# Performance work log

Hardware: AMD Instinct MI355X
Metric: run time of the kernel (lower is better)

Reference implementation:

```python
import jax, jax.numpy as jnp
import numpy as np

DIM = 512
HEADS = 8
DIM_HEAD = 64
INNER = HEADS * DIM_HEAD  # 512
EPS = 1e-5
SCALE = DIM_HEAD ** (-0.5)


def setup_inputs() -> dict:
    key = jax.random.key(0)
    ks = jax.random.split(key, 12)
    B, S = 8, 1024
    x = jax.random.normal(ks[0], (B, DIM, S, 1), dtype=jnp.float32)
    # BatchNorm2d params (eval mode: running stats)
    bn_gamma = jax.random.normal(ks[1], (DIM,), dtype=jnp.float32) * 0.1 + 1.0
    bn_beta = jax.random.normal(ks[2], (DIM,), dtype=jnp.float32) * 0.1
    bn_mean = jax.random.normal(ks[3], (DIM,), dtype=jnp.float32) * 0.1
    bn_var = jax.random.uniform(ks[4], (DIM,), dtype=jnp.float32, minval=0.5, maxval=1.5)
    # 1x1 Conv2d == linear: weight [out, in], bias [out]
    def lin(k, out_d, in_d):
        kw, kb = jax.random.split(k)
        lim = 1.0 / np.sqrt(in_d)
        w = jax.random.uniform(kw, (out_d, in_d), dtype=jnp.float32, minval=-lim, maxval=lim)
        b = jax.random.uniform(kb, (out_d,), dtype=jnp.float32, minval=-lim, maxval=lim)
        return w, b
    wq, bq = lin(ks[5], INNER, DIM)
    wk, bk = lin(ks[6], INNER, DIM)
    wv, bv = lin(ks[7], INNER, DIM)
    wo, bo = lin(ks[8], DIM, INNER)
    return {"x": x, "bn_gamma": bn_gamma, "bn_beta": bn_beta,
            "bn_mean": bn_mean, "bn_var": bn_var,
            "wq": wq, "bq": bq, "wk": wk, "bk": bk,
            "wv": wv, "bv": bv, "wo": wo, "bo": bo}


def reference(x, bn_gamma, bn_beta, bn_mean, bn_var,
              wq, bq, wk, bk, wv, bv, wo, bo):
    B, C, S, _ = x.shape
    # BatchNorm2d (eval) over channel dim
    inv = jax.lax.rsqrt(bn_var + EPS)
    xn = (x - bn_mean[None, :, None, None]) * (bn_gamma * inv)[None, :, None, None] \
         + bn_beta[None, :, None, None]
    t = jnp.transpose(xn[..., 0], (0, 2, 1))  # [B, S, C]
    q = (t @ wq.T + bq).reshape(B, S, HEADS, DIM_HEAD)
    k = (t @ wk.T + bk).reshape(B, S, HEADS, DIM_HEAD)
    v = (t @ wv.T + bv).reshape(B, S, HEADS, DIM_HEAD)
    scores = jnp.einsum('bshd,bthd->bhst', q, k) * SCALE  # [B,H,S,S]
    attn = jax.nn.softmax(scores, axis=-1)
    o = jnp.einsum('bhst,bthd->bshd', attn, v).reshape(B, S, INNER)
    y = o @ wo.T + bo  # [B, S, C]
    return jnp.transpose(y, (0, 2, 1))[..., None]  # [B, C, S, 1]
```

## Files before the change

kernel.cpp:

```cpp
#include <hip/hip_runtime.h>
#include <stdint.h>

typedef __bf16 bf16;
typedef bf16 bf16x8 __attribute__((ext_vector_type(8)));
typedef bf16 bf16x4 __attribute__((ext_vector_type(4)));
typedef float f32x4 __attribute__((ext_vector_type(4)));

#define NB 8
#define NS 1024
#define NC 512
#define NH 8
#define ND 64

#define QSCALE 0.18033688011f

__device__ __forceinline__ void gload16(const void* g, void* l) {
  __builtin_amdgcn_global_load_lds(
      (const __attribute__((address_space(1))) void*)g,
      (__attribute__((address_space(3))) void*)l, 16, 0, 0);
}

__global__ __launch_bounds__(256) void bn_tr_kernel(
    const float* __restrict__ x, const float* __restrict__ gam,
    const float* __restrict__ bet, const float* __restrict__ mu,
    const float* __restrict__ var, bf16* __restrict__ t) {
  __shared__ float tile[32][33];
  const int b = blockIdx.z, c0 = blockIdx.y * 32, s0 = blockIdx.x * 32;
  const int tx = threadIdx.x, sj = tx & 31, ci = tx >> 5;
#pragma unroll
  for (int kk = 0; kk < 4; ++kk) {
    const int c = c0 + ci + (kk << 3);
    const float sc = gam[c] * rsqrtf(var[c] + 1e-5f);
    const float sh = bet[c] - mu[c] * sc;
    tile[ci + (kk << 3)][sj] = x[(size_t)(b * NC + c) * NS + s0 + sj] * sc + sh;
  }
  __syncthreads();
#pragma unroll
  for (int kk = 0; kk < 4; ++kk) {
    const int s = s0 + ci + (kk << 3);
    t[(size_t)(b * NS + s) * NC + c0 + sj] = (bf16)tile[sj][ci + (kk << 3)];
  }
}

__global__ __launch_bounds__(256) void wconv_kernel(
    const float* __restrict__ wq, const float* __restrict__ wk,
    const float* __restrict__ wv, const float* __restrict__ wo,
    bf16* __restrict__ wqb, bf16* __restrict__ wkb, bf16* __restrict__ wvb,
    bf16* __restrict__ wob) {
  const int i = (blockIdx.x * 256 + threadIdx.x) * 4;
  float4 a = *(const float4*)(&wq[i]);
  float4 b = *(const float4*)(&wk[i]);
  float4 c = *(const float4*)(&wv[i]);
  float4 d = *(const float4*)(&wo[i]);
  bf16x4 av = {(bf16)a.x, (bf16)a.y, (bf16)a.z, (bf16)a.w};
  bf16x4 bv = {(bf16)b.x, (bf16)b.y, (bf16)b.z, (bf16)b.w};
  bf16x4 cv = {(bf16)c.x, (bf16)c.y, (bf16)c.z, (bf16)c.w};
  bf16x4 dv = {(bf16)d.x, (bf16)d.y, (bf16)d.z, (bf16)d.w};
  *(bf16x4*)(&wqb[i]) = av;
  *(bf16x4*)(&wkb[i]) = bv;
  *(bf16x4*)(&wvb[i]) = cv;
  *(bf16x4*)(&wob[i]) = dv;
}

__global__ __launch_bounds__(256) void gemm_qkv_kernel(
    const bf16* __restrict__ t, const bf16* __restrict__ wqb,
    const bf16* __restrict__ wkb, const bf16* __restrict__ wvb,
    const float* __restrict__ bq, const float* __restrict__ bk,
    const float* __restrict__ bv, bf16* __restrict__ qo, bf16* __restrict__ ko,
    bf16* __restrict__ vo) {
  __shared__ __align__(16) bf16 As[2][128 * 32];
  __shared__ __align__(16) bf16 Bs[2][128 * 32];
  const int lid = blockIdx.x;
  const int xcd = lid & 7, rr = lid >> 3;
  const int ny = rr % 12, mx = (rr / 12) * 8 + xcd;
  const int m0 = mx << 7, n0 = ny << 7;
  const int tid = threadIdx.x;
  const int wsel = n0 >> 9;
  const bf16* W = (wsel == 0) ? wqb : (wsel == 1 ? wkb : wvb);
  const float* bias = (wsel == 0) ? bq : (wsel == 1 ? bk : bv);
  const int nb = n0 & 511;
  const int w = tid >> 6, lane = tid & 63, l15 = lane & 15, l4 = lane >> 4;
  const int wm = (w >> 1) << 6, wn = (w & 1) << 6;

  const int srl = lane >> 2, sp = lane & 3;
  const int r0 = w * 16 + srl, r1 = 64 + w * 16 + srl;
  const int c0off = (sp ^ ((r0 >> 1) & 3)) << 3;
  const int c1off = (sp ^ ((r1 >> 1) & 3)) << 3;
  const bf16* a0 = t + (size_t)(m0 + r0) * 512 + c0off;
  const bf16* a1 = t + (size_t)(m0 + r1) * 512 + c1off;
  const bf16* b0 = W + (size_t)(nb + r0) * 512 + c0off;
  const bf16* b1 = W + (size_t)(nb + r1) * 512 + c1off;

  f32x4 acc[4][4] = {};
  gload16(a0, &As[0][w * 512]);
  gload16(a1, &As[0][2048 + w * 512]);
  gload16(b0, &Bs[0][w * 512]);
  gload16(b1, &Bs[0][2048 + w * 512]);
  __syncthreads();
  int buf = 0;
  for (int k0 = 0; k0 < 512; k0 += 32, buf ^= 1) {
    if (k0 + 32 < 512) {
      gload16(a0 + k0 + 32, &As[buf ^ 1][w * 512]);
      gload16(a1 + k0 + 32, &As[buf ^ 1][2048 + w * 512]);
      gload16(b0 + k0 + 32, &Bs[buf ^ 1][w * 512]);
      gload16(b1 + k0 + 32, &Bs[buf ^ 1][2048 + w * 512]);
    }
    bf16x8 af[4], bfv[4];
#pragma unroll
    for (int mi = 0; mi < 4; ++mi) {
      const int row = wm + mi * 16 + l15;
      af[mi] = *(const bf16x8*)(&As[buf][row * 32 + ((l4 ^ ((row >> 1) & 3)) << 3)]);
    }
#pragma unroll
    for (int ni = 0; ni < 4; ++ni) {
      const int row = wn + ni * 16 + l15;
      bfv[ni] = *(const bf16x8*)(&Bs[buf][row * 32 + ((l4 ^ ((row >> 1) & 3)) << 3)]);
    }
    if (wsel == 2) {
#pragma unroll
      for (int mi = 0; mi < 4; ++mi)
#pragma unroll
        for (int ni = 0; ni < 4; ++ni)
          acc[mi][ni] = __builtin_amdgcn_mfma_f32_16x16x32_bf16(
              af[mi], bfv[ni], acc[mi][ni], 0, 0, 0);
    } else {
#pragma unroll
      for (int mi = 0; mi < 4; ++mi)
#pragma unroll
        for (int ni = 0; ni < 4; ++ni)
          acc[mi][ni] = __builtin_amdgcn_mfma_f32_16x16x32_bf16(
              bfv[ni], af[mi], acc[mi][ni], 0, 0, 0);
    }
    __syncthreads();
  }
  const int bidx = m0 >> 10;
  if (wsel == 2) {
    const int sbase = (m0 & 1023) + wm + (l4 << 2);
#pragma unroll
    for (int ni = 0; ni < 4; ++ni) {
      const int nn = nb + wn + ni * 16 + l15;
      const int hh = nn >> 6, dd = nn & 63;
      const float bsv = bias[nn];
      bf16* vbase = vo + (size_t)(bidx * NH + hh) * (ND * NS) + (size_t)dd * NS + sbase;
#pragma unroll
      for (int mi = 0; mi < 4; ++mi) {
        bf16x4 pk;
#pragma unroll
        for (int r = 0; r < 4; ++r) pk[r] = (bf16)(acc[mi][ni][r] + bsv);
        *(bf16x4*)(&vbase[mi * 16]) = pk;
      }
    }
  } else {
    const bool isq = (wsel == 0);
    bf16* outp = isq ? qo : ko;
    const int sbase = (m0 & 1023) + wm + l15;
#pragma unroll
    for (int ni = 0; ni < 4; ++ni) {
      const int nn0 = nb + wn + ni * 16 + (l4 << 2);
      const int hh = nn0 >> 6, dd0 = nn0 & 63;
      const float4 bs4 = *(const float4*)(&bias[nn0]);
      bf16* obase = outp + (size_t)(bidx * NH + hh) * (NS * ND) + dd0;
#pragma unroll
      for (int mi = 0; mi < 4; ++mi) {
        bf16x4 pk;
        const float* bp = (const float*)&bs4;
#pragma unroll
        for (int r = 0; r < 4; ++r) {
          float val = acc[mi][ni][r] + bp[r];
          if (isq) val *= QSCALE;
          pk[r] = (bf16)val;
        }
        *(bf16x4*)(&obase[(size_t)(sbase + mi * 16) * ND]) = pk;
      }
    }
  }
}

__global__ __launch_bounds__(512, 4) void attn_kernel(
    const bf16* __restrict__ qg, const bf16* __restrict__ kg,
    const bf16* __restrict__ vtg, bf16* __restrict__ og) {
  __shared__ __align__(16) bf16 Kb[2][64 * 64];
  __shared__ __align__(16) bf16 Vb[2][64 * 64];
  __shared__ __align__(16) bf16 Ps[8][16 * 64];
  const int lid = blockIdx.x;
  const int xcd = lid & 7, rr = lid >> 3;
  const int bh = ((rr & 7) << 3) + xcd;
  const int q0 = (rr >> 3) << 7;
  const int tid = threadIdx.x, w = tid >> 6, lane = tid & 63;
  const int l15 = lane & 15, l4 = lane >> 4, l7 = l15 & 7;
  const bf16* Qp = qg + ((size_t)bh * NS + q0) * ND;
  const bf16* Kp = kg + (size_t)bh * NS * ND;
  const bf16* Vp = vtg + (size_t)bh * ND * NS;

  bf16x8 qf[2];
#pragma unroll
  for (int kk = 0; kk < 2; ++kk)
    qf[kk] = *(const bf16x8*)(&Qp[(size_t)(w * 16 + l15) * ND + ((kk << 2) + l4) * 8]);

  const int srow = w * 8 + (lane >> 3);
  const int scol = ((lane & 7) ^ (srow & 7)) << 3;
  const bf16* ksrc = Kp + (size_t)srow * ND + scol;
  const bf16* vsrc = Vp + (size_t)srow * NS + scol;

  f32x4 oacc[4] = {};
  float mrun = -1e30f, lrun = 0.f;

  gload16(ksrc, &Kb[0][w * 512]);
  gload16(vsrc, &Vb[0][w * 512]);
  __syncthreads();

  int buf = 0;
  for (int kv0 = 0; kv0 < NS; kv0 += 64, buf ^= 1) {
    if (kv0 + 64 < NS) {
      gload16(ksrc + (size_t)(kv0 + 64) * ND, &Kb[buf ^ 1][w * 512]);
      gload16(vsrc + (kv0 + 64), &Vb[buf ^ 1][w * 512]);
    }
    const bf16* Ks = Kb[buf];
    const bf16* Vs = Vb[buf];
    f32x4 st[4];
    __builtin_amdgcn_s_setprio(1);
#pragma unroll
    for (int rt = 0; rt < 4; ++rt) {
      const int rb = (rt * 16 + l15) * 64;
      const bf16x8 a0 = *(const bf16x8*)(&Ks[rb + ((l4 ^ l7) << 3)]);
      const bf16x8 a1 = *(const bf16x8*)(&Ks[rb + (((4 + l4) ^ l7) << 3)]);
      f32x4 z = {0.f, 0.f, 0.f, 0.f};
      z = __builtin_amdgcn_mfma_f32_16x16x32_bf16(a0, qf[0], z, 0, 0, 0);
      st[rt] = __builtin_amdgcn_mfma_f32_16x16x32_bf16(a1, qf[1], z, 0, 0, 0);
    }
    __builtin_amdgcn_s_setprio(0);
    float pm = -1e30f;
#pragma unroll
    for (int rt = 0; rt < 4; ++rt)
#pragma unroll
      for (int r = 0; r < 4; ++r) pm = fmaxf(pm, st[rt][r]);
    pm = fmaxf(pm, __shfl_xor(pm, 16));
    pm = fmaxf(pm, __shfl_xor(pm, 32));
    if (!__all(pm - mrun <= 8.f)) {
      const float mnew = fmaxf(mrun, pm);
      const float alpha = __builtin_amdgcn_exp2f(mrun - mnew);
#pragma unroll
      for (int di = 0; di < 4; ++di)
#pragma unroll
        for (int r = 0; r < 4; ++r) oacc[di][r] *= alpha;
      lrun *= alpha;
      mrun = mnew;
    }
    float rs = 0.f;
#pragma unroll
    for (int rt = 0; rt < 4; ++rt) {
      bf16x4 pk;
#pragma unroll
      for (int r = 0; r < 4; ++r) {
        const float p = __builtin_amdgcn_exp2f(st[rt][r] - mrun);
        rs += p;
        pk[r] = (bf16)p;
      }
      const int slot = (rt << 1) + (l4 >> 1);
      *(bf16x4*)(&Ps[w][l15 * 64 + ((slot ^ l7) << 3) + ((l4 & 1) << 2)]) = pk;
    }
    lrun += rs;
    const bf16x8 pa0 = *(const bf16x8*)(&Ps[w][l15 * 64 + ((l4 ^ l7) << 3)]);
    const bf16x8 pa1 = *(const bf16x8*)(&Ps[w][l15 * 64 + (((4 + l4) ^ l7) << 3)]);
    __builtin_amdgcn_s_setprio(1);
#pragma unroll
    for (int di = 0; di < 4; ++di) {
      const int vb = (di * 16 + l15) * 64;
      const bf16x8 v0 = *(const bf16x8*)(&Vs[vb + ((l4 ^ l7) << 3)]);
      const bf16x8 v1 = *(const bf16x8*)(&Vs[vb + (((4 + l4) ^ l7) << 3)]);
      oacc[di] = __builtin_amdgcn_mfma_f32_16x16x32_bf16(v0, pa0, oacc[di], 0, 0, 0);
      oacc[di] = __builtin_amdgcn_mfma_f32_16x16x32_bf16(v1, pa1, oacc[di], 0, 0, 0);
    }
    __builtin_amdgcn_s_setprio(0);
    __syncthreads();
  }
  lrun += __shfl_xor(lrun, 16);
  lrun += __shfl_xor(lrun, 32);
  const float linv = 1.f / lrun;
  const int b = bh >> 3, h = bh & 7;
  bf16* Op = og + (size_t)(b * NS + q0 + w * 16 + l15) * NC + h * ND + (l4 << 2);
#pragma unroll
  for (int di = 0; di < 4; ++di) {
    bf16x4 pk;
#pragma unroll
    for (int r = 0; r < 4; ++r) pk[r] = (bf16)(oacc[di][r] * linv);
    *(bf16x4*)(&Op[di * 16]) = pk;
  }
}

__global__ __launch_bounds__(256) void gemm_out_kernel(
    const bf16* __restrict__ wob, const bf16* __restrict__ o,
    const float* __restrict__ bo, float* __restrict__ out) {
  __shared__ __align__(16) bf16 As[2][128 * 32];
  __shared__ __align__(16) bf16 Bs[2][128 * 32];
  const int lid = blockIdx.x;
  const int xcd = lid & 7, rr = lid >> 3;
  const int mx = rr & 3, ny = ((rr >> 2) << 3) + xcd;
  const int m0 = mx << 7, n0 = ny << 7;
  const int tid = threadIdx.x;
  const int w = tid >> 6, lane = tid & 63, l15 = lane & 15, l4 = lane >> 4;
  const int wm = (w >> 1) << 6, wn = (w & 1) << 6;

  const int srl = lane >> 2, sp = lane & 3;
  const int r0 = w * 16 + srl, r1 = 64 + w * 16 + srl;
  const int c0off = (sp ^ ((r0 >> 1) & 3)) << 3;
  const int c1off = (sp ^ ((r1 >> 1) & 3)) << 3;
  const bf16* a0 = wob + (size_t)(m0 + r0) * 512 + c0off;
  const bf16* a1 = wob + (size_t)(m0 + r1) * 512 + c1off;
  const bf16* b0 = o + (size_t)(n0 + r0) * 512 + c0off;
  const bf16* b1 = o + (size_t)(n0 + r1) * 512 + c1off;

  f32x4 acc[4][4] = {};
  gload16(a0, &As[0][w * 512]);
  gload16(a1, &As[0][2048 + w * 512]);
  gload16(b0, &Bs[0][w * 512]);
  gload16(b1, &Bs[0][2048 + w * 512]);
  __syncthreads();
  int buf = 0;
  for (int k0 = 0; k0 < 512; k0 += 32, buf ^= 1) {
    if (k0 + 32 < 512) {
      gload16(a0 + k0 + 32, &As[buf ^ 1][w * 512]);
      gload16(a1 + k0 + 32, &As[buf ^ 1][2048 + w * 512]);
      gload16(b0 + k0 + 32, &Bs[buf ^ 1][w * 512]);
      gload16(b1 + k0 + 32, &Bs[buf ^ 1][2048 + w * 512]);
    }
    bf16x8 af[4], bfv[4];
#pragma unroll
    for (int mi = 0; mi < 4; ++mi) {
      const int row = wm + mi * 16 + l15;
      af[mi] = *(const bf16x8*)(&As[buf][row * 32 + ((l4 ^ ((row >> 1) & 3)) << 3)]);
    }
#pragma unroll
    for (int ni = 0; ni < 4; ++ni) {
      const int row = wn + ni * 16 + l15;
      bfv[ni] = *(const bf16x8*)(&Bs[buf][row * 32 + ((l4 ^ ((row >> 1) & 3)) << 3)]);
    }
#pragma unroll
    for (int mi = 0; mi < 4; ++mi)
#pragma unroll
      for (int ni = 0; ni < 4; ++ni)
        acc[mi][ni] = __builtin_amdgcn_mfma_f32_16x16x32_bf16(
            bfv[ni], af[mi], acc[mi][ni], 0, 0, 0);
    __syncthreads();
  }
  const int b = n0 >> 10;
  const int sb = (n0 & 1023) + wn;
#pragma unroll
  for (int mi = 0; mi < 4; ++mi) {
    const int cout = m0 + wm + mi * 16 + l15;
    const float bsv = bo[cout];
    float* obase = out + (size_t)(b * NC + cout) * NS;
#pragma unroll
    for (int ni = 0; ni < 4; ++ni) {
      const int s0i = sb + ni * 16 + (l4 << 2);
      float4 pk = {acc[mi][ni][0] + bsv, acc[mi][ni][1] + bsv,
                   acc[mi][ni][2] + bsv, acc[mi][ni][3] + bsv};
      *(float4*)(&obase[s0i]) = pk;
    }
  }
}

extern "C" void kernel_launch(void* const* d_in, const int* in_sizes, int n_in,
                              void* d_out, int out_size, void* d_ws,
                              size_t ws_size, hipStream_t stream) {
  const float* x = (const float*)d_in[0];
  const float* gam = (const float*)d_in[1];
  const float* bet = (const float*)d_in[2];
  const float* mu = (const float*)d_in[3];
  const float* var = (const float*)d_in[4];
  const float* wq = (const float*)d_in[5];
  const float* bq = (const float*)d_in[6];
  const float* wk = (const float*)d_in[7];
  const float* bk = (const float*)d_in[8];
  const float* wv = (const float*)d_in[9];
  const float* bv = (const float*)d_in[10];
  const float* wo = (const float*)d_in[11];
  const float* bo = (const float*)d_in[12];
  float* out = (float*)d_out;

  char* p = (char*)d_ws;
  const size_t big = (size_t)8192 * 512 * sizeof(bf16);
  bf16* t = (bf16*)p;   p += big;
  bf16* q = (bf16*)p;   p += big;
  bf16* k = (bf16*)p;   p += big;
  bf16* vt = (bf16*)p;  p += big;
  const size_t wsz = (size_t)512 * 512 * sizeof(bf16);
  bf16* wqb = (bf16*)p; p += wsz;
  bf16* wkb = (bf16*)p; p += wsz;
  bf16* wvb = (bf16*)p; p += wsz;
  bf16* wob = (bf16*)p; p += wsz;
  bf16* o = t;

  bn_tr_kernel<<<dim3(32, 16, 8), 256, 0, stream>>>(x, gam, bet, mu, var, t);
  wconv_kernel<<<dim3(256), 256, 0, stream>>>(wq, wk, wv, wo, wqb, wkb, wvb, wob);
  gemm_qkv_kernel<<<dim3(768), 256, 0, stream>>>(t, wqb, wkb, wvb, bq, bk, bv,
                                                 q, k, vt);
  attn_kernel<<<dim3(512), 512, 0, stream>>>(q, k, vt, o);
  gemm_out_kernel<<<dim3(256), 256, 0, stream>>>(wob, o, bo, out);
}
```

Baseline: 87.91 us.

## Merge prep kernels, widen attention KV tile to 128, halve out-GEMM M tile

Merges the batchnorm-transpose and weight-conversion kernels into one launch, which saves a kernel launch. The attention kernel now processes 128 keys per iteration with double-buffered K/V tiles, and PV is interleaved per 32-key chunk through a smaller P scratch. This halves the loop trip count and the barrier count but raises LDS use per block. The output GEMM uses 64x128 tiles with 512 blocks to fill more CUs, at the cost of less data reuse per block.

```diff
diff --git a/kernel.cpp b/kernel.cpp
--- a/kernel.cpp
+++ b/kernel.cpp
@@ -20,46 +20,46 @@
       (__attribute__((address_space(3))) void*)l, 16, 0, 0);
 }
 
-__global__ __launch_bounds__(256) void bn_tr_kernel(
+__global__ __launch_bounds__(256) void prep_kernel(
     const float* __restrict__ x, const float* __restrict__ gam,
     const float* __restrict__ bet, const float* __restrict__ mu,
-    const float* __restrict__ var, bf16* __restrict__ t) {
+    const float* __restrict__ var, const float* __restrict__ wq,
+    const float* __restrict__ wk, const float* __restrict__ wv,
+    const float* __restrict__ wo, bf16* __restrict__ t, bf16* __restrict__ wqb,
+    bf16* __restrict__ wkb, bf16* __restrict__ wvb, bf16* __restrict__ wob) {
   __shared__ float tile[32][33];
-  const int b = blockIdx.z, c0 = blockIdx.y * 32, s0 = blockIdx.x * 32;
-  const int tx = threadIdx.x, sj = tx & 31, ci = tx >> 5;
-#pragma unroll
-  for (int kk = 0; kk < 4; ++kk) {
-    const int c = c0 + ci + (kk << 3);
-    const float sc = gam[c] * rsqrtf(var[c] + 1e-5f);
-    const float sh = bet[c] - mu[c] * sc;
-    tile[ci + (kk << 3)][sj] = x[(size_t)(b * NC + c) * NS + s0 + sj] * sc + sh;
-  }
-  __syncthreads();
-#pragma unroll
-  for (int kk = 0; kk < 4; ++kk) {
-    const int s = s0 + ci + (kk << 3);
-    t[(size_t)(b * NS + s) * NC + c0 + sj] = (bf16)tile[sj][ci + (kk << 3)];
-  }
-}
-
-__global__ __launch_bounds__(256) void wconv_kernel(
-    const float* __restrict__ wq, const float* __restrict__ wk,
-    const float* __restrict__ wv, const float* __restrict__ wo,
-    bf16* __restrict__ wqb, bf16* __restrict__ wkb, bf16* __restrict__ wvb,
-    bf16* __restrict__ wob) {
-  const int i = (blockIdx.x * 256 + threadIdx.x) * 4;
-  float4 a = *(const float4*)(&wq[i]);
-  float4 b = *(const float4*)(&wk[i]);
-  float4 c = *(const float4*)(&wv[i]);
-  float4 d = *(const float4*)(&wo[i]);
-  bf16x4 av = {(bf16)a.x, (bf16)a.y, (bf16)a.z, (bf16)a.w};
-  bf16x4 bv = {(bf16)b.x, (bf16)b.y, (bf16)b.z, (bf16)b.w};
-  bf16x4 cv = {(bf16)c.x, (bf16)c.y, (bf16)c.z, (bf16)c.w};
-  bf16x4 dv = {(bf16)d.x, (bf16)d.y, (bf16)d.z, (bf16)d.w};
-  *(bf16x4*)(&wqb[i]) = av;
-  *(bf16x4*)(&wkb[i]) = bv;
-  *(bf16x4*)(&wvb[i]) = cv;
-  *(bf16x4*)(&wob[i]) = dv;
+  const int bid = blockIdx.x;
+  if (bid < 4096) {
+    const int b = bid >> 9, c0 = ((bid >> 5) & 15) << 5, s0 = (bid & 31) << 5;
+    const int tx = threadIdx.x, sj = tx & 31, ci = tx >> 5;
+#pragma unroll
+    for (int kk = 0; kk < 4; ++kk) {
+      const int c = c0 + ci + (kk << 3);
+      const float sc = gam[c] * rsqrtf(var[c] + 1e-5f);
+      const float sh = bet[c] - mu[c] * sc;
+      tile[ci + (kk << 3)][sj] = x[(size_t)(b * NC + c) * NS + s0 + sj] * sc + sh;
+    }
+    __syncthreads();
+#pragma unroll
+    for (int kk = 0; kk < 4; ++kk) {
+      const int s = s0 + ci + (kk << 3);
+      t[(size_t)(b * NS + s) * NC + c0 + sj] = (bf16)tile[sj][ci + (kk << 3)];
+    }
+  } else {
+    const int i = ((bid - 4096) * 256 + threadIdx.x) * 4;
+    float4 a = *(const float4*)(&wq[i]);
+    float4 b = *(const float4*)(&wk[i]);
+    float4 c = *(const float4*)(&wv[i]);
+    float4 d = *(const float4*)(&wo[i]);
+    bf16x4 av = {(bf16)a.x, (bf16)a.y, (bf16)a.z, (bf16)a.w};
+    bf16x4 bv = {(bf16)b.x, (bf16)b.y, (bf16)b.z, (bf16)b.w};
+    bf16x4 cv = {(bf16)c.x, (bf16)c.y, (bf16)c.z, (bf16)c.w};
+    bf16x4 dv = {(bf16)d.x, (bf16)d.y, (bf16)d.z, (bf16)d.w};
+    *(bf16x4*)(&wqb[i]) = av;
+    *(bf16x4*)(&wkb[i]) = bv;
+    *(bf16x4*)(&wvb[i]) = cv;
+    *(bf16x4*)(&wob[i]) = dv;
+  }
 }
 
 __global__ __launch_bounds__(256) void gemm_qkv_kernel(
@@ -179,15 +179,15 @@
 __global__ __launch_bounds__(512, 4) void attn_kernel(
     const bf16* __restrict__ qg, const bf16* __restrict__ kg,
     const bf16* __restrict__ vtg, bf16* __restrict__ og) {
-  __shared__ __align__(16) bf16 Kb[2][64 * 64];
-  __shared__ __align__(16) bf16 Vb[2][64 * 64];
-  __shared__ __align__(16) bf16 Ps[8][16 * 64];
+  __shared__ __align__(16) bf16 Kb[2][128 * 64];
+  __shared__ __align__(16) bf16 Vb[2][64 * 128];
+  __shared__ __align__(16) bf16 Ps[8][16 * 40];
   const int lid = blockIdx.x;
   const int xcd = lid & 7, rr = lid >> 3;
   const int bh = ((rr & 7) << 3) + xcd;
   const int q0 = (rr >> 3) << 7;
   const int tid = threadIdx.x, w = tid >> 6, lane = tid & 63;
-  const int l15 = lane & 15, l4 = lane >> 4, l7 = l15 & 7;
+  const int l15 = lane & 15, l4 = lane >> 4;
   const bf16* Qp = qg + ((size_t)bh * NS + q0) * ND;
   const bf16* Kp = kg + (size_t)bh * NS * ND;
   const bf16* Vp = vtg + (size_t)bh * ND * NS;
@@ -197,43 +197,50 @@
   for (int kk = 0; kk < 2; ++kk)
     qf[kk] = *(const bf16x8*)(&Qp[(size_t)(w * 16 + l15) * ND + ((kk << 2) + l4) * 8]);
 
-  const int srow = w * 8 + (lane >> 3);
-  const int scol = ((lane & 7) ^ (srow & 7)) << 3;
-  const bf16* ksrc = Kp + (size_t)srow * ND + scol;
-  const bf16* vsrc = Vp + (size_t)srow * NS + scol;
+  const int krow = w * 16 + (lane >> 3);
+  const bf16* ksrc = Kp + (size_t)krow * ND + (((lane & 7) ^ (krow & 7)) << 3);
+  const int vrow1 = w * 8 + (lane >> 4);
+  const int vrow2 = vrow1 + 4;
+  const bf16* vsrc1 = Vp + (size_t)vrow1 * NS + (((lane & 15) ^ (vrow1 & 7)) << 3);
+  const bf16* vsrc2 = Vp + (size_t)vrow2 * NS + (((lane & 15) ^ (vrow2 & 7)) << 3);
 
   f32x4 oacc[4] = {};
   float mrun = -1e30f, lrun = 0.f;
 
-  gload16(ksrc, &Kb[0][w * 512]);
-  gload16(vsrc, &Vb[0][w * 512]);
+  gload16(ksrc, &Kb[0][w * 1024]);
+  gload16(ksrc + 8 * ND, &Kb[0][w * 1024 + 512]);
+  gload16(vsrc1, &Vb[0][w * 1024]);
+  gload16(vsrc2, &Vb[0][w * 1024 + 512]);
   __syncthreads();
 
   int buf = 0;
-  for (int kv0 = 0; kv0 < NS; kv0 += 64, buf ^= 1) {
-    if (kv0 + 64 < NS) {
-      gload16(ksrc + (size_t)(kv0 + 64) * ND, &Kb[buf ^ 1][w * 512]);
-      gload16(vsrc + (kv0 + 64), &Vb[buf ^ 1][w * 512]);
+  for (int kv0 = 0; kv0 < NS; kv0 += 128, buf ^= 1) {
+    if (kv0 + 128 < NS) {
+      gload16(ksrc + (size_t)(kv0 + 128) * ND, &Kb[buf ^ 1][w * 1024]);
+      gload16(ksrc + (size_t)(kv0 + 136) * ND, &Kb[buf ^ 1][w * 1024 + 512]);
+      gload16(vsrc1 + kv0 + 128, &Vb[buf ^ 1][w * 1024]);
+      gload16(vsrc2 + kv0 + 128, &Vb[buf ^ 1][w * 1024 + 512]);
     }
     const bf16* Ks = Kb[buf];
     const bf16* Vs = Vb[buf];
-    f32x4 st[4];
+    f32x4 st[8];
     __builtin_amdgcn_s_setprio(1);
 #pragma unroll
-    for (int rt = 0; rt < 4; ++rt) {
-      const int rb = (rt * 16 + l15) * 64;
-      const bf16x8 a0 = *(const bf16x8*)(&Ks[rb + ((l4 ^ l7) << 3)]);
-      const bf16x8 a1 = *(const bf16x8*)(&Ks[rb + (((4 + l4) ^ l7) << 3)]);
+    for (int rt = 0; rt < 8; ++rt) {
+      const int row = rt * 16 + l15;
+      const int rb = row * 64, s = row & 7;
+      const bf16x8 a0 = *(const bf16x8*)(&Ks[rb + ((l4 ^ s) << 3)]);
+      const bf16x8 a1 = *(const bf16x8*)(&Ks[rb + (((4 + l4) ^ s) << 3)]);
       f32x4 z = {0.f, 0.f, 0.f, 0.f};
       z = __builtin_amdgcn_mfma_f32_16x16x32_bf16(a0, qf[0], z, 0, 0, 0);
       st[rt] = __builtin_amdgcn_mfma_f32_16x16x32_bf16(a1, qf[1], z, 0, 0, 0);
     }
     __builtin_amdgcn_s_setprio(0);
-    float pm = -1e30f;
-#pragma unroll
-    for (int rt = 0; rt < 4; ++rt)
-#pragma unroll
-      for (int r = 0; r < 4; ++r) pm = fmaxf(pm, st[rt][r]);
+    float pm = fmaxf(fmaxf(st[0][0], st[0][1]), fmaxf(st[0][2], st[0][3]));
+#pragma unroll
+    for (int rt = 1; rt < 8; ++rt)
+      pm = fmaxf(pm, fmaxf(fmaxf(st[rt][0], st[rt][1]),
+                           fmaxf(st[rt][2], st[rt][3])));
     pm = fmaxf(pm, __shfl_xor(pm, 16));
     pm = fmaxf(pm, __shfl_xor(pm, 32));
     if (!__all(pm - mrun <= 8.f)) {
@@ -247,31 +254,33 @@
       mrun = mnew;
     }
     float rs = 0.f;
-#pragma unroll
-    for (int rt = 0; rt < 4; ++rt) {
-      bf16x4 pk;
+    bf16* prow = &Ps[w][l15 * 40];
+#pragma unroll
+    for (int c = 0; c < 4; ++c) {
+      bf16x4 pk1, pk2;
 #pragma unroll
       for (int r = 0; r < 4; ++r) {
-        const float p = __builtin_amdgcn_exp2f(st[rt][r] - mrun);
-        rs += p;
-        pk[r] = (bf16)p;
+        const float p1 = __builtin_amdgcn_exp2f(st[2 * c][r] - mrun);
+        const float p2 = __builtin_amdgcn_exp2f(st[2 * c + 1][r] - mrun);
+        rs += p1 + p2;
+        pk1[r] = (bf16)p1;
+        pk2[r] = (bf16)p2;
       }
-      const int slot = (rt << 1) + (l4 >> 1);
-      *(bf16x4*)(&Ps[w][l15 * 64 + ((slot ^ l7) << 3) + ((l4 & 1) << 2)]) = pk;
+      *(bf16x4*)(&prow[4 * l4]) = pk1;
+      *(bf16x4*)(&prow[16 + 4 * l4]) = pk2;
+      const bf16x8 pa = *(const bf16x8*)(&prow[l4 * 8]);
+      __builtin_amdgcn_s_setprio(1);
+#pragma unroll
+      for (int di = 0; di < 4; ++di) {
+        const int vrow = di * 16 + l15;
+        const int slot = (c << 2) + l4;
+        const bf16x8 vf =
+            *(const bf16x8*)(&Vs[vrow * 128 + ((slot ^ (vrow & 7)) << 3)]);
+        oacc[di] = __builtin_amdgcn_mfma_f32_16x16x32_bf16(vf, pa, oacc[di], 0, 0, 0);
+      }
+      __builtin_amdgcn_s_setprio(0);
     }
     lrun += rs;
-    const bf16x8 pa0 = *(const bf16x8*)(&Ps[w][l15 * 64 + ((l4 ^ l7) << 3)]);
-    const bf16x8 pa1 = *(const bf16x8*)(&Ps[w][l15 * 64 + (((4 + l4) ^ l7) << 3)]);
-    __builtin_amdgcn_s_setprio(1);
-#pragma unroll
-    for (int di = 0; di < 4; ++di) {
-      const int vb = (di * 16 + l15) * 64;
-      const bf16x8 v0 = *(const bf16x8*)(&Vs[vb + ((l4 ^ l7) << 3)]);
-      const bf16x8 v1 = *(const bf16x8*)(&Vs[vb + (((4 + l4) ^ l7) << 3)]);
-      oacc[di] = __builtin_amdgcn_mfma_f32_16x16x32_bf16(v0, pa0, oacc[di], 0, 0, 0);
-      oacc[di] = __builtin_amdgcn_mfma_f32_16x16x32_bf16(v1, pa1, oacc[di], 0, 0, 0);
-    }
-    __builtin_amdgcn_s_setprio(0);
     __syncthreads();
   }
   lrun += __shfl_xor(lrun, 16);
@@ -291,28 +300,29 @@
 __global__ __launch_bounds__(256) void gemm_out_kernel(
     const bf16* __restrict__ wob, const bf16* __restrict__ o,
     const float* __restrict__ bo, float* __restrict__ out) {
-  __shared__ __align__(16) bf16 As[2][128 * 32];
+  __shared__ __align__(16) bf16 As[2][64 * 32];
   __shared__ __align__(16) bf16 Bs[2][128 * 32];
   const int lid = blockIdx.x;
   const int xcd = lid & 7, rr = lid >> 3;
-  const int mx = rr & 3, ny = ((rr >> 2) << 3) + xcd;
-  const int m0 = mx << 7, n0 = ny << 7;
+  const int mx = rr & 7, ny = ((rr >> 3) << 3) + xcd;
+  const int m0 = mx << 6, n0 = ny << 7;
   const int tid = threadIdx.x;
   const int w = tid >> 6, lane = tid & 63, l15 = lane & 15, l4 = lane >> 4;
-  const int wm = (w >> 1) << 6, wn = (w & 1) << 6;
+  const int wm = (w >> 1) << 5;
+  const int wn = (w & 1) << 6;
 
   const int srl = lane >> 2, sp = lane & 3;
-  const int r0 = w * 16 + srl, r1 = 64 + w * 16 + srl;
-  const int c0off = (sp ^ ((r0 >> 1) & 3)) << 3;
-  const int c1off = (sp ^ ((r1 >> 1) & 3)) << 3;
-  const bf16* a0 = wob + (size_t)(m0 + r0) * 512 + c0off;
-  const bf16* a1 = wob + (size_t)(m0 + r1) * 512 + c1off;
-  const bf16* b0 = o + (size_t)(n0 + r0) * 512 + c0off;
-  const bf16* b1 = o + (size_t)(n0 + r1) * 512 + c1off;
-
-  f32x4 acc[4][4] = {};
+  const int ra = w * 16 + srl;
+  const int caoff = (sp ^ ((ra >> 1) & 3)) << 3;
+  const bf16* a0 = wob + (size_t)(m0 + ra) * 512 + caoff;
+  const int rb0 = w * 16 + srl, rb1 = 64 + w * 16 + srl;
+  const int cb0off = (sp ^ ((rb0 >> 1) & 3)) << 3;
+  const int cb1off = (sp ^ ((rb1 >> 1) & 3)) << 3;
+  const bf16* b0 = o + (size_t)(n0 + rb0) * 512 + cb0off;
+  const bf16* b1 = o + (size_t)(n0 + rb1) * 512 + cb1off;
+
+  f32x4 acc[2][4] = {};
   gload16(a0, &As[0][w * 512]);
-  gload16(a1, &As[0][2048 + w * 512]);
   gload16(b0, &Bs[0][w * 512]);
   gload16(b1, &Bs[0][2048 + w * 512]);
   __syncthreads();
@@ -320,13 +330,12 @@
   for (int k0 = 0; k0 < 512; k0 += 32, buf ^= 1) {
     if (k0 + 32 < 512) {
       gload16(a0 + k0 + 32, &As[buf ^ 1][w * 512]);
-      gload16(a1 + k0 + 32, &As[buf ^ 1][2048 + w * 512]);
       gload16(b0 + k0 + 32, &Bs[buf ^ 1][w * 512]);
       gload16(b1 + k0 + 32, &Bs[buf ^ 1][2048 + w * 512]);
     }
-    bf16x8 af[4], bfv[4];
-#pragma unroll
-    for (int mi = 0; mi < 4; ++mi) {
+    bf16x8 af[2], bfv[4];
+#pragma unroll
+    for (int mi = 0; mi < 2; ++mi) {
       const int row = wm + mi * 16 + l15;
       af[mi] = *(const bf16x8*)(&As[buf][row * 32 + ((l4 ^ ((row >> 1) & 3)) << 3)]);
     }
@@ -336,7 +345,7 @@
       bfv[ni] = *(const bf16x8*)(&Bs[buf][row * 32 + ((l4 ^ ((row >> 1) & 3)) << 3)]);
     }
 #pragma unroll
-    for (int mi = 0; mi < 4; ++mi)
+    for (int mi = 0; mi < 2; ++mi)
 #pragma unroll
       for (int ni = 0; ni < 4; ++ni)
         acc[mi][ni] = __builtin_amdgcn_mfma_f32_16x16x32_bf16(
@@ -346,7 +355,7 @@
   const int b = n0 >> 10;
   const int sb = (n0 & 1023) + wn;
 #pragma unroll
-  for (int mi = 0; mi < 4; ++mi) {
+  for (int mi = 0; mi < 2; ++mi) {
     const int cout = m0 + wm + mi * 16 + l15;
     const float bsv = bo[cout];
     float* obase = out + (size_t)(b * NC + cout) * NS;
@@ -391,10 +400,10 @@
   bf16* wob = (bf16*)p; p += wsz;
   bf16* o = t;
 
-  bn_tr_kernel<<<dim3(32, 16, 8), 256, 0, stream>>>(x, gam, bet, mu, var, t);
-  wconv_kernel<<<dim3(256), 256, 0, stream>>>(wq, wk, wv, wo, wqb, wkb, wvb, wob);
+  prep_kernel<<<dim3(4352), 256, 0, stream>>>(x, gam, bet, mu, var, wq, wk, wv,
+                                              wo, t, wqb, wkb, wvb, wob);
   gemm_qkv_kernel<<<dim3(768), 256, 0, stream>>>(t, wqb, wkb, wvb, bq, bk, bv,
                                                  q, k, vt);
   attn_kernel<<<dim3(512), 512, 0, stream>>>(q, k, vt, o);
-  gemm_out_kernel<<<dim3(256), 256, 0, stream>>>(wob, o, bo, out);
-}
+  gemm_out_kernel<<<dim3(512), 256, 0, stream>>>(wob, o, bo, out);
+}
```

After: 87.27 us. About the same (-0.7%).
